# Performance work log

Measured on AMD Instinct MI355X. Metric: run time of the kernel, lower is better.

Reference implementation:

```python
import jax, jax.numpy as jnp
import numpy as np

EMBED, HEADS, LEVELS, POINTS = 256, 8, 3, 4
HD = EMBED // HEADS
SHAPES = [(200, 200), (100, 100), (50, 50)]


def layer_norm(x, g, b, eps=1e-5):
    m = x.mean(-1, keepdims=True)
    v = ((x - m) ** 2).mean(-1, keepdims=True)
    return (x - m) * jax.lax.rsqrt(v + eps) * g + b


def bilinear_sample(v, loc, H, W):
    """v: (bs, H*W, heads, hd); loc: (bs, nq, heads, P, 2) normalized to [0,1].
    Matches F.grid_sample(bilinear, align_corners=False, padding_mode='zeros')
    applied to grid = 2*loc - 1. Returns (bs, nq, heads, P, hd)."""
    bs, nq, heads, P, _ = loc.shape
    hd = v.shape[-1]
    x = loc[..., 0] * W - 0.5
    y = loc[..., 1] * H - 0.5
    x0 = jnp.floor(x); y0 = jnp.floor(y)
    tx = x - x0; ty = y - y0
    x0i = x0.astype(jnp.int32); y0i = y0.astype(jnp.int32)
    vT = v.transpose(0, 2, 1, 3)  # (bs, heads, HW, hd)
    out = jnp.zeros((bs, heads, nq * P, hd), v.dtype)
    for dy, wy in ((0, 1.0 - ty), (1, ty)):
        for dx, wx in ((0, 1.0 - tx), (1, tx)):
            xi = x0i + dx; yi = y0i + dy
            valid = (xi >= 0) & (xi < W) & (yi >= 0) & (yi < H)
            idx = jnp.clip(yi, 0, H - 1) * W + jnp.clip(xi, 0, W - 1)
            w = (wx * wy * valid).transpose(0, 2, 1, 3).reshape(bs, heads, nq * P)
            idxT = idx.transpose(0, 2, 1, 3).reshape(bs, heads, nq * P)
            g = jnp.take_along_axis(vT, idxT[..., None], axis=2)  # (bs,heads,nqP,hd)
            out = out + w[..., None] * g
    return out.reshape(bs, heads, nq, P, hd).transpose(0, 2, 1, 3, 4)


def reference(query, value, query_pos, ref_pts, spatial_shapes, level_start_index,
              norm1_g, norm1_b, W_off, b_off, W_attn, b_attn, W_val, b_val,
              W_out, b_out, norm2_g, norm2_b, W1, b1, W2, b2):
    shapes = np.asarray(spatial_shapes)
    bs, nq, _ = query.shape
    # --- MultiScaleDeformableAttention on norm1(query) ---
    q = layer_norm(query, norm1_g, norm1_b)
    identity = q
    qp = q + query_pos
    offsets = (qp @ W_off + b_off).reshape(bs, nq, HEADS, LEVELS, POINTS, 2)
    aw = (qp @ W_attn + b_attn).reshape(bs, nq, HEADS, LEVELS * POINTS)
    aw = jax.nn.softmax(aw, axis=-1).reshape(bs, nq, HEADS, LEVELS, POINTS)
    v = (value @ W_val + b_val).reshape(bs, -1, HEADS, HD)
    # offset normalizer is (W, H) per level
    normalizer = jnp.stack([spatial_shapes[:, 1], spatial_shapes[:, 0]], -1).astype(query.dtype)
    loc = ref_pts[:, :, None, :, None, :] + offsets / normalizer[None, None, None, :, None, :]
    out = jnp.zeros((bs, nq, HEADS, HD), query.dtype)
    start = 0
    for l in range(LEVELS):
        H, W = int(shapes[l, 0]), int(shapes[l, 1])
        vl = v[:, start:start + H * W]
        s = bilinear_sample(vl, loc[:, :, :, l], H, W)  # (bs,nq,heads,P,hd)
        out = out + jnp.einsum('bqhpd,bqhp->bqhd', s, aw[:, :, :, l])
        start += H * W
    attn_out = out.reshape(bs, nq, EMBED) @ W_out + b_out + identity
    x = query + attn_out
    # --- FFN ---
    h = layer_norm(x, norm2_g, norm2_b)
    ffn = jax.nn.gelu(h @ W1 + b1, approximate=False) @ W2 + b2
    return x + ffn


def setup_inputs() -> dict:
    key = jax.random.key(0)
    ks = jax.random.split(key, 16)
    bs, nq = 1, 40000
    nv = sum(h * w for h, w in SHAPES)
    d = EMBED
    inp = {
        'query': jax.random.normal(ks[0], (bs, nq, d), jnp.float32),
        'value': jax.random.normal(ks[1], (bs, nv, d), jnp.float32),
        'query_pos': jax.random.normal(ks[2], (bs, nq, d), jnp.float32),
        'ref_pts': jax.random.uniform(ks[3], (bs, nq, LEVELS, 2), jnp.float32),
        'spatial_shapes': jnp.array(SHAPES, dtype=jnp.int32),
        'level_start_index': jnp.array(np.cumsum([0] + [h * w for h, w in SHAPES[:-1]]), dtype=jnp.int32),
    }
    s = 1.0 / np.sqrt(d)
    inp.update({
        'norm1_g': jnp.ones((d,), jnp.float32), 'norm1_b': jnp.zeros((d,), jnp.float32),
        'W_off': jax.random.normal(ks[4], (d, HEADS * LEVELS * POINTS * 2), jnp.float32) * 0.01,
        'b_off': jax.random.normal(ks[5], (HEADS * LEVELS * POINTS * 2,), jnp.float32) * 0.5,
        'W_attn': jax.random.normal(ks[6], (d, HEADS * LEVELS * POINTS), jnp.float32) * s,
        'b_attn': jnp.zeros((HEADS * LEVELS * POINTS,), jnp.float32),
        'W_val': jax.random.normal(ks[7], (d, d), jnp.float32) * s,
        'b_val': jnp.zeros((d,), jnp.float32),
        'W_out': jax.random.normal(ks[8], (d, d), jnp.float32) * s,
        'b_out': jnp.zeros((d,), jnp.float32),
        'norm2_g': jnp.ones((d,), jnp.float32), 'norm2_b': jnp.zeros((d,), jnp.float32),
        'W1': jax.random.normal(ks[9], (d, 4 * d), jnp.float32) * s,
        'b1': jnp.zeros((4 * d,), jnp.float32),
        'W2': jax.random.normal(ks[10], (4 * d, d), jnp.float32) / np.sqrt(4 * d),
        'b2': jnp.zeros((d,), jnp.float32),
    })
    return inp
```

## Files before the change

kernel.cpp:

```cpp
#include <hip/hip_runtime.h>
#include <hip/hip_bf16.h>
#include <math.h>

#define NQ 40000
#define NV 52500
#define D 256
#define NHEAD 8
#define HD 32
#define GUARD 256

using bf16x8 = __attribute__((ext_vector_type(8))) short;
using f32x4  = __attribute__((ext_vector_type(4))) float;
typedef int v2i32 __attribute__((ext_vector_type(2)));

__device__ __forceinline__ short f2bf(float f) {
  union { __hip_bfloat16 h; short s; } u;
  u.h = __float2bfloat16(f);
  return u.s;
}
__device__ __forceinline__ float bf2f(unsigned short s) {
  return __uint_as_float((unsigned)s << 16);
}
__device__ __forceinline__ unsigned pack2(float lo, float hi) {
  return (unsigned)(unsigned short)f2bf(lo) |
         ((unsigned)(unsigned short)f2bf(hi) << 16);
}
__device__ __forceinline__ void gload16(const void* g, void* l) {
  __builtin_amdgcn_global_load_lds(
      (const __attribute__((address_space(1))) unsigned int*)g,
      (__attribute__((address_space(3))) unsigned int*)l, 16, 0, 0);
}

template<int IMM>
__device__ __forceinline__ float swz_add(float x) {
  return x + __int_as_float(__builtin_amdgcn_ds_swizzle(__float_as_int(x), IMM));
}

__global__ __launch_bounds__(256) void k_prep(const float* __restrict__ Woff,
                                              const float* __restrict__ Wattn,
                                              const float* __restrict__ Wval,
                                              const float* __restrict__ Wout,
                                              const float* __restrict__ W1,
                                              const float* __restrict__ W2,
                                              const float* __restrict__ boff,
                                              const float* __restrict__ battn,
                                              short* __restrict__ WT288,
                                              short* __restrict__ WTval,
                                              short* __restrict__ WTout,
                                              short* __restrict__ WT1,
                                              short* __restrict__ WT2,
                                              float* __restrict__ bias288) {
  int idx = blockIdx.x * 256 + threadIdx.x;
  if (idx < 49152) {
    int n = idx >> 8, k = idx & 255;
    WT288[idx] = f2bf(Woff[k * 192 + n]);
  } else if (idx < 73728) {
    int li = idx - 49152; int n = li >> 8, k = li & 255;
    WT288[49152 + li] = f2bf(Wattn[k * 96 + n]);
  } else if (idx < 139264) {
    int li = idx - 73728; int n = li >> 8, k = li & 255;
    WTval[li] = f2bf(Wval[k * 256 + n]);
  } else if (idx < 204800) {
    int li = idx - 139264; int n = li >> 8, k = li & 255;
    WTout[li] = f2bf(Wout[k * 256 + n]);
  } else if (idx < 466944) {
    int li = idx - 204800; int n = li >> 8, k = li & 255;
    WT1[li] = f2bf(W1[k * 1024 + n]);
  } else if (idx < 729088) {
    int li = idx - 466944; int n = li >> 10, k = li & 1023;
    WT2[li] = f2bf(W2[k * 256 + n]);
  } else if (idx < 729376) {
    int i = idx - 729088;
    bias288[i] = (i < 192) ? boff[i] : battn[i - 192];
  }
}

__global__ __launch_bounds__(256) void k_ln1(const float* __restrict__ qin,
                                             const float* __restrict__ qpos,
                                             const float* __restrict__ g,
                                             const float* __restrict__ b,
                                             short* __restrict__ id_out,
                                             short* __restrict__ qp_out) {
  int wave = threadIdx.x >> 6;
  int lane = threadIdx.x & 63;
  int row  = blockIdx.x * 4 + wave;
  float4 x = ((const float4*)(qin + (size_t)row * D))[lane];
  float s  = x.x + x.y + x.z + x.w;
  float ss = x.x*x.x + x.y*x.y + x.z*x.z + x.w*x.w;
  for (int o = 32; o > 0; o >>= 1) { s += __shfl_down(s, o); ss += __shfl_down(ss, o); }
  s  = __shfl(s, 0);
  ss = __shfl(ss, 0);
  float m   = s * (1.0f / 256.0f);
  float var = ss * (1.0f / 256.0f) - m * m;
  float rs  = rsqrtf(var + 1e-5f);
  float4 gg = ((const float4*)g)[lane];
  float4 bb = ((const float4*)b)[lane];
  float4 qn;
  qn.x = (x.x - m) * rs * gg.x + bb.x;
  qn.y = (x.y - m) * rs * gg.y + bb.y;
  qn.z = (x.z - m) * rs * gg.z + bb.z;
  qn.w = (x.w - m) * rs * gg.w + bb.w;
  short4 io;
  io.x = f2bf(qn.x); io.y = f2bf(qn.y); io.z = f2bf(qn.z); io.w = f2bf(qn.w);
  ((short4*)(id_out + (size_t)row * D))[lane] = io;
  float4 p = ((const float4*)(qpos + (size_t)row * D))[lane];
  short4 o;
  o.x = f2bf(qn.x + p.x); o.y = f2bf(qn.y + p.y);
  o.z = f2bf(qn.z + p.z); o.w = f2bf(qn.w + p.w);
  ((short4*)(qp_out + (size_t)row * D))[lane] = o;
}

__global__ __launch_bounds__(256) void k_ln2(const float* __restrict__ xin,
                                             const float* __restrict__ g,
                                             const float* __restrict__ b,
                                             short* __restrict__ h_out) {
  int wave = threadIdx.x >> 6;
  int lane = threadIdx.x & 63;
  int row  = blockIdx.x * 4 + wave;
  float4 x = ((const float4*)(xin + (size_t)row * D))[lane];
  float s  = x.x + x.y + x.z + x.w;
  float ss = x.x*x.x + x.y*x.y + x.z*x.z + x.w*x.w;
  for (int o = 32; o > 0; o >>= 1) { s += __shfl_down(s, o); ss += __shfl_down(ss, o); }
  s  = __shfl(s, 0);
  ss = __shfl(ss, 0);
  float m   = s * (1.0f / 256.0f);
  float var = ss * (1.0f / 256.0f) - m * m;
  float rs  = rsqrtf(var + 1e-5f);
  float4 gg = ((const float4*)g)[lane];
  float4 bb = ((const float4*)b)[lane];
  short4 o;
  o.x = f2bf((x.x - m) * rs * gg.x + bb.x);
  o.y = f2bf((x.y - m) * rs * gg.y + bb.y);
  o.z = f2bf((x.z - m) * rs * gg.z + bb.z);
  o.w = f2bf((x.w - m) * rs * gg.w + bb.w);
  ((short4*)(h_out + (size_t)row * D))[lane] = o;
}

template<int EPI, int CVTA, int K>
__global__ __launch_bounds__(256) void k_gemm(const void* __restrict__ Ain,
                                              const short* __restrict__ WT,
                                              const float* __restrict__ bias,
                                              float* __restrict__ Cf,
                                              short* __restrict__ Cb,
                                              const float* __restrict__ R1,
                                              const float* __restrict__ R2,
                                              int M, int N) {
  constexpr int NT = K / 32;
  __shared__ short Al[3][4096];
  __shared__ short Bl[3][4096];
  const int tid = threadIdx.x;

  const int nbx = gridDim.x;
  const int nwg = nbx * gridDim.y;
  int flat = blockIdx.y * nbx + blockIdx.x;
  {
    int xcd = flat & 7, pos = flat >> 3;
    int qq = nwg >> 3, rr = nwg & 7;
    flat = (xcd < rr ? xcd * (qq + 1) : rr * (qq + 1) + (xcd - rr) * qq) + pos;
  }
  const int n0 = (flat % nbx) * 128, m0 = (flat / nbx) * 128;

  const int w = tid >> 6, l = tid & 63;
  const int wm = (w >> 1) * 64, wn = (w & 1) * 64;
  const int lr = l & 15;

  const int c0s = w * 2, c1s = c0s + 1;
  const int sr = l >> 2;
  const int sg = (((l & 3) ^ ((l >> 3) & 3)) << 3);
  const int ar0 = min(m0 + c0s * 16 + sr, M - 1);
  const int ar1 = min(m0 + c1s * 16 + sr, M - 1);
  const int br0 = min(n0 + c0s * 16 + sr, N - 1);
  const int br1 = min(n0 + c1s * 16 + sr, N - 1);
  const short* bP0 = WT + (size_t)br0 * K + sg;
  const short* bP1 = WT + (size_t)br1 * K + sg;
  const short* aP0 = (const short*)Ain + (size_t)ar0 * K + sg;
  const short* aP1 = (const short*)Ain + (size_t)ar1 * K + sg;
  const float* aF0 = (const float*)Ain + (size_t)ar0 * K + sg;
  const float* aF1 = (const float*)Ain + (size_t)ar1 * K + sg;
  short* wD0 = &Al[0][(c0s * 16 + sr) * 32 + ((l & 3) << 3)];
  short* wD1 = &Al[0][(c1s * 16 + sr) * 32 + ((l & 3) << 3)];

  const int fsw = (((l >> 4) ^ ((l >> 1) & 3)) << 3);
  const int aRd = (wm + lr) * 32 + fsw;
  const int bRd = (wn + lr) * 32 + fsw;

  f32x4 acc[4][4];
#pragma unroll
  for (int i = 0; i < 4; ++i)
#pragma unroll
    for (int j = 0; j < 4; ++j) acc[i][j] = (f32x4){0, 0, 0, 0};

  if (CVTA) {
    {
      float4 f00 = *(const float4*)(aF0);
      float4 f01 = *(const float4*)(aF0 + 4);
      float4 f10 = *(const float4*)(aF1);
      float4 f11 = *(const float4*)(aF1 + 4);
      int4 p0, p1;
      p0.x = pack2(f00.x, f00.y); p0.y = pack2(f00.z, f00.w);
      p0.z = pack2(f01.x, f01.y); p0.w = pack2(f01.z, f01.w);
      p1.x = pack2(f10.x, f10.y); p1.y = pack2(f10.z, f10.w);
      p1.z = pack2(f11.x, f11.y); p1.w = pack2(f11.z, f11.w);
      *(int4*)wD0 = p0;
      *(int4*)wD1 = p1;
      gload16(bP0, &Bl[0][c0s * 512]);
      gload16(bP1, &Bl[0][c1s * 512]);
      __syncthreads();
    }
#pragma unroll 2
    for (int t = 0; t < NT - 1; ++t) {
      const int buf = t & 1, nbuf = buf ^ 1;
      const int kn = (t + 1) * 32;
      float4 f00 = *(const float4*)(aF0 + kn);
      float4 f01 = *(const float4*)(aF0 + kn + 4);
      float4 f10 = *(const float4*)(aF1 + kn);
      float4 f11 = *(const float4*)(aF1 + kn + 4);
      gload16(bP0 + kn, &Bl[nbuf][c0s * 512]);
      gload16(bP1 + kn, &Bl[nbuf][c1s * 512]);

      bf16x8 af[4], bfr[4];
#pragma unroll
      for (int i = 0; i < 4; ++i) {
        af[i]  = *(const bf16x8*)&Al[buf][aRd + i * 512];
        bfr[i] = *(const bf16x8*)&Bl[buf][bRd + i * 512];
      }
#pragma unroll
      for (int i = 0; i < 4; ++i)
#pragma unroll
        for (int j = 0; j < 4; ++j)
          acc[i][j] = __builtin_amdgcn_mfma_f32_16x16x32_bf16(af[i], bfr[j], acc[i][j], 0, 0, 0);

      int4 p0, p1;
      p0.x = pack2(f00.x, f00.y); p0.y = pack2(f00.z, f00.w);
      p0.z = pack2(f01.x, f01.y); p0.w = pack2(f01.z, f01.w);
      p1.x = pack2(f10.x, f10.y); p1.y = pack2(f10.z, f10.w);
      p1.z = pack2(f11.x, f11.y); p1.w = pack2(f11.z, f11.w);
      *(int4*)(wD0 + nbuf * 4096) = p0;
      *(int4*)(wD1 + nbuf * 4096) = p1;
      __syncthreads();
    }
    {
      const int buf = (NT - 1) & 1;
      bf16x8 af[4], bfr[4];
#pragma unroll
      for (int i = 0; i < 4; ++i) {
        af[i]  = *(const bf16x8*)&Al[buf][aRd + i * 512];
        bfr[i] = *(const bf16x8*)&Bl[buf][bRd + i * 512];
      }
#pragma unroll
      for (int i = 0; i < 4; ++i)
#pragma unroll
        for (int j = 0; j < 4; ++j)
          acc[i][j] = __builtin_amdgcn_mfma_f32_16x16x32_bf16(af[i], bfr[j], acc[i][j], 0, 0, 0);
    }
  } else {
    gload16(aP0, &Al[0][c0s * 512]);
    gload16(aP1, &Al[0][c1s * 512]);
    gload16(bP0, &Bl[0][c0s * 512]);
    gload16(bP1, &Bl[0][c1s * 512]);
    if (NT > 1) {
      gload16(aP0 + 32, &Al[1][c0s * 512]);
      gload16(aP1 + 32, &Al[1][c1s * 512]);
      gload16(bP0 + 32, &Bl[1][c0s * 512]);
      gload16(bP1 + 32, &Bl[1][c1s * 512]);
    }
#pragma unroll
    for (int t = 0; t < NT; ++t) {
      const int buf = t % 3;
      if (t + 1 < NT) asm volatile("s_waitcnt vmcnt(4)" ::: "memory");
      else            asm volatile("s_waitcnt vmcnt(0)" ::: "memory");
      __builtin_amdgcn_s_barrier();
      __builtin_amdgcn_sched_barrier(0);
      if (t + 2 < NT) {
        const int kn = (t + 2) * 32, nb = (t + 2) % 3;
        gload16(aP0 + kn, &Al[nb][c0s * 512]);
        gload16(aP1 + kn, &Al[nb][c1s * 512]);
        gload16(bP0 + kn, &Bl[nb][c0s * 512]);
        gload16(bP1 + kn, &Bl[nb][c1s * 512]);
      }
      bf16x8 af[4], bfr[4];
#pragma unroll
      for (int i = 0; i < 4; ++i) {
        af[i]  = *(const bf16x8*)&Al[buf][aRd + i * 512];
        bfr[i] = *(const bf16x8*)&Bl[buf][bRd + i * 512];
      }
#pragma unroll
      for (int i = 0; i < 4; ++i)
#pragma unroll
        for (int j = 0; j < 4; ++j)
          acc[i][j] = __builtin_amdgcn_mfma_f32_16x16x32_bf16(af[i], bfr[j], acc[i][j], 0, 0, 0);
    }
  }

  __syncthreads();
  float* scratch = (float*)&Al[0][0];
  const unsigned short* R2b = (const unsigned short*)R2;
  const int wrow = (w >> 1) * 16;
  const int rl2 = tid >> 3;
  const int cc0 = (tid & 7) * 16;
  const bool colok = (n0 + cc0) < N;
  float bsv[16];
#pragma unroll
  for (int c = 0; c < 4; ++c) {
    float4 bv = {0, 0, 0, 0};
    if (colok) bv = *(const float4*)&bias[n0 + cc0 + c * 4];
    bsv[c*4+0] = bv.x; bsv[c*4+1] = bv.y; bsv[c*4+2] = bv.z; bsv[c*4+3] = bv.w;
  }
#pragma unroll
  for (int i = 0; i < 4; ++i) {
#pragma unroll
    for (int j = 0; j < 4; ++j) {
      const int col = wn + j * 16 + (l & 15);
      const int rbase = wrow + ((l >> 4) << 2);
#pragma unroll
      for (int r = 0; r < 4; ++r)
        scratch[(rbase + r) * 140 + col] = acc[i][j][r];
    }
    __syncthreads();
    const int grow = m0 + 16 * i + (rl2 < 16 ? rl2 : 48 + rl2);
    if (colok && grow < M) {
      const size_t base = (size_t)grow * N + n0 + cc0;
      float v16[16];
#pragma unroll
      for (int c = 0; c < 4; ++c) {
        float4 vv = *(const float4*)&scratch[rl2 * 140 + cc0 + c * 4];
        v16[c*4+0] = vv.x + bsv[c*4+0];
        v16[c*4+1] = vv.y + bsv[c*4+1];
        v16[c*4+2] = vv.z + bsv[c*4+2];
        v16[c*4+3] = vv.w + bsv[c*4+3];
      }
      if (EPI == 0) {
#pragma unroll
        for (int c = 0; c < 4; ++c)
          *(float4*)&Cf[base + c * 4] =
              (float4){v16[c*4], v16[c*4+1], v16[c*4+2], v16[c*4+3]};
      } else if (EPI == 1) {
        unsigned pk[8];
#pragma unroll
        for (int c = 0; c < 8; ++c) {
          float a0 = v16[2*c], a1 = v16[2*c+1];
          float u0 = a0 * (2.3021178f + 0.1029445f * a0 * a0);
          float u1 = a1 * (2.3021178f + 0.1029445f * a1 * a1);
          float g0 = a0 - a0 / (1.0f + exp2f(u0));
          float g1 = a1 - a1 / (1.0f + exp2f(u1));
          pk[c] = pack2(g0, g1);
        }
        *(uint4*)&Cb[base] = (uint4){pk[0], pk[1], pk[2], pk[3]};
        *(uint4*)&Cb[base + 8] = (uint4){pk[4], pk[5], pk[6], pk[7]};
      } else if (EPI == 5) {
        uint4 rb0 = *(const uint4*)&R2b[base];
        uint4 rb1 = *(const uint4*)&R2b[base + 8];
        unsigned rw[8] = {rb0.x, rb0.y, rb0.z, rb0.w, rb1.x, rb1.y, rb1.z, rb1.w};
        float r2v[16];
#pragma unroll
        for (int c = 0; c < 8; ++c) {
          r2v[2*c]   = __uint_as_float(rw[c] << 16);
          r2v[2*c+1] = __uint_as_float(rw[c] & 0xffff0000u);
        }
#pragma unroll
        for (int c = 0; c < 4; ++c) {
          float4 r1 = *(const float4*)&R1[base + c * 4];
          *(float4*)&Cf[base + c * 4] =
              (float4){v16[c*4] + r1.x + r2v[c*4], v16[c*4+1] + r1.y + r2v[c*4+1],
                       v16[c*4+2] + r1.z + r2v[c*4+2], v16[c*4+3] + r1.w + r2v[c*4+3]};
        }
      } else if (EPI == 3) {
#pragma unroll
        for (int c = 0; c < 4; ++c) {
          float4 cur = *(const float4*)&Cf[base + c * 4];
          *(float4*)&Cf[base + c * 4] =
              (float4){cur.x + v16[c*4], cur.y + v16[c*4+1],
                       cur.z + v16[c*4+2], cur.w + v16[c*4+3]};
        }
      } else {
        uint4 o0 = (uint4){pack2(v16[0], v16[1]), pack2(v16[2], v16[3]),
                           pack2(v16[4], v16[5]), pack2(v16[6], v16[7])};
        uint4 o1 = (uint4){pack2(v16[8], v16[9]), pack2(v16[10], v16[11]),
                           pack2(v16[12], v16[13]), pack2(v16[14], v16[15])};
        *(uint4*)&Cb[base] = o0;
        *(uint4*)&Cb[base + 8] = o1;
      }
    }
    __syncthreads();
  }
}

__global__ __launch_bounds__(256) void k_post(const unsigned short* __restrict__ res,
                                              const float* __restrict__ refp,
                                              int* __restrict__ idxA,
                                              unsigned short* __restrict__ wA) {
  int t = blockIdx.x * 256 + threadIdx.x;
  if (t >= NQ * 8) return;
  int q = t >> 3, h = t & 7;
  const unsigned short* rr = res + (size_t)q * 288;
  const unsigned short* lg = rr + 192 + h * 12;
  float lf[12];
#pragma unroll
  for (int i = 0; i < 12; ++i) lf[i] = bf2f(lg[i]);
  float mx = lf[0];
#pragma unroll
  for (int i = 1; i < 12; ++i) mx = fmaxf(mx, lf[i]);
  float e[12]; float sum = 0.0f;
#pragma unroll
  for (int i = 0; i < 12; ++i) { e[i] = expf(lf[i] - mx); sum += e[i]; }
  float inv = 1.0f / sum;

  const float dims[3] = {200.0f, 100.0f, 50.0f};
  const int   sts[3]  = {0, 40000, 50000};
#pragma unroll
  for (int l = 0; l < 3; ++l) {
    const int W = (int)dims[l];
    const float fW = dims[l];
    float rx = refp[((size_t)q * 3 + l) * 2 + 0];
    float ry = refp[((size_t)q * 3 + l) * 2 + 1];
    float invd = 1.0f / fW;
#pragma unroll
    for (int p = 0; p < 4; ++p) {
      int j = ((h * 3 + l) * 4 + p) * 2;
      float lx = rx + bf2f(rr[j + 0]) * invd;
      float ly = ry + bf2f(rr[j + 1]) * invd;
      float fx = lx * fW - 0.5f;
      float fy = ly * fW - 0.5f;
      float x0f = floorf(fx), y0f = floorf(fy);
      float tx = fx - x0f, ty = fy - y0f;
      int x0 = (int)x0f, y0 = (int)y0f;
      bool vx0 = (unsigned)x0       < (unsigned)W;
      bool vx1 = (unsigned)(x0 + 1) < (unsigned)W;
      bool vy0 = (unsigned)y0       < (unsigned)W;
      bool vy1 = (unsigned)(y0 + 1) < (unsigned)W;
      float a = e[l * 4 + p] * inv;
      float w00 = (vx0 && vy0) ? a * (1.0f - tx) * (1.0f - ty) : 0.0f;
      float w01 = (vx1 && vy0) ? a * tx * (1.0f - ty) : 0.0f;
      float w10 = (vx0 && vy1) ? a * (1.0f - tx) * ty : 0.0f;
      float w11 = (vx1 && vy1) ? a * tx * ty : 0.0f;
      int pidx = t * 12 + l * 4 + p;
      idxA[pidx] = sts[l] + y0 * W + x0;
      short4 wpk;
      wpk.x = f2bf(w00); wpk.y = f2bf(w01);
      wpk.z = f2bf(w10); wpk.w = f2bf(w11);
      *(short4*)(wA + (size_t)pidx * 4) = wpk;
    }
  }
}

__global__ __launch_bounds__(256) void k_sample(const short* __restrict__ vprojG,
                                                const int* __restrict__ idxA,
                                                const unsigned short* __restrict__ wA,
                                                short* __restrict__ smp) {
  const int lane = threadIdx.x & 63;
  const int qh   = blockIdx.x * 16 + (threadIdx.x >> 6) * 4 + (lane >> 4);
  const int tap  = (lane >> 2) & 3;
  const int cq   = lane & 3;
  const int h = qh & 7;
  const int dy = tap >> 1, dx = tap & 1;
  const short* vb = vprojG + (size_t)GUARD * D + h * HD + cq * 8;
  const int pbase = qh * 12;

  float acc[8];
#pragma unroll
  for (int j = 0; j < 8; ++j) acc[j] = 0.0f;

  const int Dim[3] = {200, 100, 50};
#pragma unroll
  for (int it = 0; it < 12; ++it) {
    const int W = Dim[it >> 2];
    const int tapoff = dy * W + dx;
    int pidx = pbase + it;
    int idx = idxA[pidx] + tapoff;
    float wgt = bf2f(wA[(size_t)pidx * 4 + tap]);
    uint4 v = *(const uint4*)(vb + (ptrdiff_t)idx * D);
    acc[0] = fmaf(wgt, __uint_as_float(v.x << 16),        acc[0]);
    acc[1] = fmaf(wgt, __uint_as_float(v.x & 0xffff0000u), acc[1]);
    acc[2] = fmaf(wgt, __uint_as_float(v.y << 16),        acc[2]);
    acc[3] = fmaf(wgt, __uint_as_float(v.y & 0xffff0000u), acc[3]);
    acc[4] = fmaf(wgt, __uint_as_float(v.z << 16),        acc[4]);
    acc[5] = fmaf(wgt, __uint_as_float(v.z & 0xffff0000u), acc[5]);
    acc[6] = fmaf(wgt, __uint_as_float(v.w << 16),        acc[6]);
    acc[7] = fmaf(wgt, __uint_as_float(v.w & 0xffff0000u), acc[7]);
  }

#pragma unroll
  for (int j = 0; j < 8; ++j) {
    float a = swz_add<0x101F>(acc[j]);
    acc[j] = swz_add<0x201F>(a);
  }

  if (tap == 0) {
    uint4 o;
    o.x = pack2(acc[0], acc[1]);
    o.y = pack2(acc[2], acc[3]);
    o.z = pack2(acc[4], acc[5]);
    o.w = pack2(acc[6], acc[7]);
    *(uint4*)(smp + (size_t)qh * HD + cq * 8) = o;
  }
}

extern "C" void kernel_launch(void* const* d_in, const int* in_sizes, int n_in,
                              void* d_out, int out_size, void* d_ws, size_t ws_size,
                              hipStream_t stream) {
  const float* query  = (const float*)d_in[0];
  const float* value  = (const float*)d_in[1];
  const float* qpos   = (const float*)d_in[2];
  const float* refp   = (const float*)d_in[3];
  const float* n1g = (const float*)d_in[6];
  const float* n1b = (const float*)d_in[7];
  const float* Woff = (const float*)d_in[8];
  const float* boff = (const float*)d_in[9];
  const float* Wattn = (const float*)d_in[10];
  const float* battn = (const float*)d_in[11];
  const float* Wval = (const float*)d_in[12];
  const float* bval = (const float*)d_in[13];
  const float* Wout = (const float*)d_in[14];
  const float* bout = (const float*)d_in[15];
  const float* n2g = (const float*)d_in[16];
  const float* n2b = (const float*)d_in[17];
  const float* W1 = (const float*)d_in[18];
  const float* b1 = (const float*)d_in[19];
  const float* W2 = (const float*)d_in[20];
  const float* b2 = (const float*)d_in[21];

  float* out = (float*)d_out;
  char* Wb = (char*)d_ws;

  short* qp_bf   = (short*)Wb;
  short* iden_bf = (short*)(Wb + 20480000);
  int*   idxA    = (int*)(Wb + 61440000);
  unsigned short* wA = (unsigned short*)(Wb + 76800000);
  short* res_bf  = (short*)(Wb + 107520000);
  short* vprjG   = (short*)(Wb + 107520000);
  short* vprj_bf = (short*)(Wb + 107520000 + GUARD * D * 2);
  short* h_bf    = (short*)(Wb + 107520000);
  short* smp_bf  = (short*)(Wb + 134662144);
  short* mid_bf  = (short*)Wb;
  char*  Wbase   = Wb + 155142144;
  short* WT288   = (short*)(Wbase);
  short* WTval   = (short*)(Wbase + 147456);
  short* WTout   = (short*)(Wbase + 278528);
  short* WT1     = (short*)(Wbase + 409600);
  short* WT2     = (short*)(Wbase + 933888);
  float* bias288 = (float*)(Wbase + 1458176);

  k_prep<<<(729376 + 255) / 256, 256, 0, stream>>>(
      Woff, Wattn, Wval, Wout, W1, W2, boff, battn,
      WT288, WTval, WTout, WT1, WT2, bias288);

  k_ln1<<<NQ / 4, 256, 0, stream>>>(query, qpos, n1g, n1b, iden_bf, qp_bf);

  k_gemm<4,0,256><<<dim3(3, (NQ + 127) / 128), 256, 0, stream>>>(
      qp_bf, WT288, bias288, nullptr, res_bf, nullptr, nullptr, NQ, 288);
  k_post<<<(NQ * 8 + 255) / 256, 256, 0, stream>>>(
      (const unsigned short*)res_bf, refp, idxA, wA);

  k_gemm<4,1,256><<<dim3(2, (NV + 127) / 128), 256, 0, stream>>>(
      value, WTval, bval, nullptr, vprj_bf, nullptr, nullptr, NV, 256);

  k_sample<<<NQ * NHEAD / 16, 256, 0, stream>>>(vprjG, idxA, wA, smp_bf);

  k_gemm<5,0,256><<<dim3(2, (NQ + 127) / 128), 256, 0, stream>>>(
      smp_bf, WTout, bout, out, nullptr, query, (const float*)iden_bf, NQ, 256);

  k_ln2<<<NQ / 4, 256, 0, stream>>>(out, n2g, n2b, h_bf);

  k_gemm<1,0,256><<<dim3(8, (NQ + 127) / 128), 256, 0, stream>>>(
      h_bf, WT1, b1, nullptr, mid_bf, nullptr, nullptr, NQ, 1024);

  k_gemm<3,0,1024><<<dim3(2, (NQ + 127) / 128), 256, 0, stream>>>(
      mid_bf, WT2, b2, out, nullptr, nullptr, nullptr, NQ, 256);
}
```

Measured before the change: 362.3 us.

## Transpose sampling index/weight layout and broadcast indices via ds_bpermute; raise MFMA priority

The per-(query,head) sampling indices are stored padded to 16 entries and the bilinear weights are stored tap-major. Each lane of k_sample now loads one index and broadcasts it with ds_bpermute, and loads its tap's 12 weights in two vector loads, instead of issuing scalar gathers every iteration. This cuts the number of global loads in the sampling kernel at the cost of extra cross-lane permutes and a larger padded index buffer. The GEMM also raises wave priority around its MFMA block, and the guard region and workspace offsets are re-laid out.

```diff
diff --git a/kernel.cpp b/kernel.cpp
--- a/kernel.cpp
+++ b/kernel.cpp
@@ -7,7 +7,7 @@
 #define D 256
 #define NHEAD 8
 #define HD 32
-#define GUARD 256
+#define GUARD 512
 
 using bf16x8 = __attribute__((ext_vector_type(8))) short;
 using f32x4  = __attribute__((ext_vector_type(4))) float;
@@ -284,11 +284,13 @@
         af[i]  = *(const bf16x8*)&Al[buf][aRd + i * 512];
         bfr[i] = *(const bf16x8*)&Bl[buf][bRd + i * 512];
       }
+      __builtin_amdgcn_s_setprio(1);
 #pragma unroll
       for (int i = 0; i < 4; ++i)
 #pragma unroll
         for (int j = 0; j < 4; ++j)
           acc[i][j] = __builtin_amdgcn_mfma_f32_16x16x32_bf16(af[i], bfr[j], acc[i][j], 0, 0, 0);
+      __builtin_amdgcn_s_setprio(0);
     }
   }
 
@@ -387,8 +389,8 @@
 
 __global__ __launch_bounds__(256) void k_post(const unsigned short* __restrict__ res,
                                               const float* __restrict__ refp,
-                                              int* __restrict__ idxA,
-                                              unsigned short* __restrict__ wA) {
+                                              int* __restrict__ idxB,
+                                              unsigned short* __restrict__ wT) {
   int t = blockIdx.x * 256 + threadIdx.x;
   if (t >= NQ * 8) return;
   int q = t >> 3, h = t & 7;
@@ -407,6 +409,8 @@
 
   const float dims[3] = {200.0f, 100.0f, 50.0f};
   const int   sts[3]  = {0, 40000, 50000};
+  int* idq = idxB + (size_t)t * 16;
+  unsigned short* wq = wT + (size_t)t * 64;
 #pragma unroll
   for (int l = 0; l < 3; ++l) {
     const int W = (int)dims[l];
@@ -433,49 +437,56 @@
       float w01 = (vx1 && vy0) ? a * tx * (1.0f - ty) : 0.0f;
       float w10 = (vx0 && vy1) ? a * (1.0f - tx) * ty : 0.0f;
       float w11 = (vx1 && vy1) ? a * tx * ty : 0.0f;
-      int pidx = t * 12 + l * 4 + p;
-      idxA[pidx] = sts[l] + y0 * W + x0;
-      short4 wpk;
-      wpk.x = f2bf(w00); wpk.y = f2bf(w01);
-      wpk.z = f2bf(w10); wpk.w = f2bf(w11);
-      *(short4*)(wA + (size_t)pidx * 4) = wpk;
+      int pt = l * 4 + p;
+      idq[pt] = sts[l] + y0 * W + x0;
+      wq[0 * 16 + pt] = (unsigned short)f2bf(w00);
+      wq[1 * 16 + pt] = (unsigned short)f2bf(w01);
+      wq[2 * 16 + pt] = (unsigned short)f2bf(w10);
+      wq[3 * 16 + pt] = (unsigned short)f2bf(w11);
     }
   }
 }
 
 __global__ __launch_bounds__(256) void k_sample(const short* __restrict__ vprojG,
-                                                const int* __restrict__ idxA,
-                                                const unsigned short* __restrict__ wA,
+                                                const int* __restrict__ idxB,
+                                                const unsigned short* __restrict__ wT,
                                                 short* __restrict__ smp) {
   const int lane = threadIdx.x & 63;
-  const int qh   = blockIdx.x * 16 + (threadIdx.x >> 6) * 4 + (lane >> 4);
+  const int slot = lane >> 4;
+  const int qh   = blockIdx.x * 16 + (threadIdx.x >> 6) * 4 + slot;
   const int tap  = (lane >> 2) & 3;
   const int cq   = lane & 3;
   const int h = qh & 7;
   const int dy = tap >> 1, dx = tap & 1;
   const short* vb = vprojG + (size_t)GUARD * D + h * HD + cq * 8;
-  const int pbase = qh * 12;
+
+  const int myidx = idxB[(size_t)qh * 16 + (lane & 15)];
+  const unsigned short* wp = wT + ((size_t)qh * 4 + tap) * 16;
+  uint4 w8 = *(const uint4*)wp;
+  uint2 w4 = *(const uint2*)(wp + 8);
+  const unsigned wd[6] = {w8.x, w8.y, w8.z, w8.w, w4.x, w4.y};
 
   float acc[8];
 #pragma unroll
   for (int j = 0; j < 8; ++j) acc[j] = 0.0f;
 
   const int Dim[3] = {200, 100, 50};
+  const int slotbase = slot << 4;
 #pragma unroll
   for (int it = 0; it < 12; ++it) {
     const int W = Dim[it >> 2];
-    const int tapoff = dy * W + dx;
-    int pidx = pbase + it;
-    int idx = idxA[pidx] + tapoff;
-    float wgt = bf2f(wA[(size_t)pidx * 4 + tap]);
+    int idx0 = __builtin_amdgcn_ds_bpermute((slotbase + it) << 2, myidx);
+    int idx = idx0 + dy * W + dx;
+    unsigned wraw = wd[it >> 1];
+    float wgt = __uint_as_float((it & 1) ? (wraw & 0xffff0000u) : (wraw << 16));
     uint4 v = *(const uint4*)(vb + (ptrdiff_t)idx * D);
-    acc[0] = fmaf(wgt, __uint_as_float(v.x << 16),        acc[0]);
+    acc[0] = fmaf(wgt, __uint_as_float(v.x << 16),         acc[0]);
     acc[1] = fmaf(wgt, __uint_as_float(v.x & 0xffff0000u), acc[1]);
-    acc[2] = fmaf(wgt, __uint_as_float(v.y << 16),        acc[2]);
+    acc[2] = fmaf(wgt, __uint_as_float(v.y << 16),         acc[2]);
     acc[3] = fmaf(wgt, __uint_as_float(v.y & 0xffff0000u), acc[3]);
-    acc[4] = fmaf(wgt, __uint_as_float(v.z << 16),        acc[4]);
+    acc[4] = fmaf(wgt, __uint_as_float(v.z << 16),         acc[4]);
     acc[5] = fmaf(wgt, __uint_as_float(v.z & 0xffff0000u), acc[5]);
-    acc[6] = fmaf(wgt, __uint_as_float(v.w << 16),        acc[6]);
+    acc[6] = fmaf(wgt, __uint_as_float(v.w << 16),         acc[6]);
     acc[7] = fmaf(wgt, __uint_as_float(v.w & 0xffff0000u), acc[7]);
   }
 
@@ -524,15 +535,15 @@
 
   short* qp_bf   = (short*)Wb;
   short* iden_bf = (short*)(Wb + 20480000);
-  int*   idxA    = (int*)(Wb + 61440000);
-  unsigned short* wA = (unsigned short*)(Wb + 76800000);
-  short* res_bf  = (short*)(Wb + 107520000);
-  short* vprjG   = (short*)(Wb + 107520000);
-  short* vprj_bf = (short*)(Wb + 107520000 + GUARD * D * 2);
-  short* h_bf    = (short*)(Wb + 107520000);
-  short* smp_bf  = (short*)(Wb + 134662144);
+  int*   idxB    = (int*)(Wb + 40960000);
+  unsigned short* wT = (unsigned short*)(Wb + 61440000);
+  short* res_bf  = (short*)(Wb + 102400000);
+  short* vprjG   = (short*)(Wb + 102400000);
+  short* vprj_bf = (short*)(Wb + 102400000 + GUARD * D * 2);
+  short* h_bf    = (short*)(Wb + 102400000);
+  short* smp_bf  = (short*)(Wb + 130000000);
   short* mid_bf  = (short*)Wb;
-  char*  Wbase   = Wb + 155142144;
+  char*  Wbase   = Wb + 150600000;
   short* WT288   = (short*)(Wbase);
   short* WTval   = (short*)(Wbase + 147456);
   short* WTout   = (short*)(Wbase + 278528);
@@ -549,12 +560,12 @@
   k_gemm<4,0,256><<<dim3(3, (NQ + 127) / 128), 256, 0, stream>>>(
       qp_bf, WT288, bias288, nullptr, res_bf, nullptr, nullptr, NQ, 288);
   k_post<<<(NQ * 8 + 255) / 256, 256, 0, stream>>>(
-      (const unsigned short*)res_bf, refp, idxA, wA);
+      (const unsigned short*)res_bf, refp, idxB, wT);
 
   k_gemm<4,1,256><<<dim3(2, (NV + 127) / 128), 256, 0, stream>>>(
       value, WTval, bval, nullptr, vprj_bf, nullptr, nullptr, NV, 256);
 
-  k_sample<<<NQ * NHEAD / 16, 256, 0, stream>>>(vprjG, idxA, wA, smp_bf);
+  k_sample<<<NQ * NHEAD / 16, 256, 0, stream>>>(vprjG, idxB, wT, smp_bf);
 
   k_gemm<5,0,256><<<dim3(2, (NQ + 127) / 128), 256, 0, stream>>>(
       smp_bf, WTout, bout, out, nullptr, query, (const float*)iden_bf, NQ, 256);
```

Result: faster. 349.7 us (-3.5%).
